# Kernel optimization log

Hardware: AMD Instinct MI355X
Metric: run time of the kernel (lower is better)

The kernel has to match this reference:

```python
import jax, jax.numpy as jnp
import numpy as np

N_HEAD = 16


def setup_inputs() -> dict:
    key = jax.random.key(0)
    ks = jax.random.split(key, 6)
    B, T, C = 2, 2048, 1024
    x = jax.random.normal(ks[0], (B, T, C), dtype=jnp.float32)
    # causal mask, broadcastable over [B, H, T, T]
    attn_mask = jnp.tril(jnp.ones((T, T), dtype=jnp.int32))[None, None]
    s = 1.0 / np.sqrt(C)
    W_attn = jax.random.normal(ks[1], (C, 3 * C), dtype=jnp.float32) * s
    b_attn = jnp.zeros((3 * C,), dtype=jnp.float32)
    W_proj = jax.random.normal(ks[2], (C, C), dtype=jnp.float32) * s
    b_proj = jnp.zeros((C,), dtype=jnp.float32)
    return {"x": x, "attn_mask": attn_mask, "W_attn": W_attn,
            "b_attn": b_attn, "W_proj": W_proj, "b_proj": b_proj}


def reference(x, attn_mask, W_attn, b_attn, W_proj, b_proj):
    B, T, C = x.shape
    H = N_HEAD
    D = C // H
    qkv = x @ W_attn + b_attn                      # [B, T, 3C]
    q, k, v = jnp.split(qkv, 3, axis=-1)
    q = q.reshape(B, T, H, D).transpose(0, 2, 1, 3)  # [B, H, T, D]
    k = k.reshape(B, T, H, D).transpose(0, 2, 1, 3)
    v = v.reshape(B, T, H, D).transpose(0, 2, 1, 3)
    att = jnp.einsum('bhtd,bhsd->bhts', q, k) * (1.0 / np.sqrt(D))
    att = jnp.where(attn_mask == 0, jnp.float32(-jnp.inf), att)
    att = jax.nn.softmax(att, axis=-1)             # [B, H, T, T]
    y = jnp.einsum('bhts,bhsd->bhtd', att, v)      # [B, H, T, D]
    y = y.transpose(0, 2, 1, 3).reshape(B, T, C)
    y = y @ W_proj + b_proj
    return y
```

## Files before the change

### kernel.cpp

```cpp
#include <hip/hip_runtime.h>
#include <hip/hip_bf16.h>
#include <stdint.h>

#define H_NUM 16
#define DH 64
#define TSEQ 2048
#define CDIM 1024

typedef short shortx8 __attribute__((ext_vector_type(8)));
typedef float f32x4 __attribute__((ext_vector_type(4)));
typedef unsigned short u16;
typedef unsigned int u32;
typedef unsigned long long u64;

#define MFMA16(a,b,c) __builtin_amdgcn_mfma_f32_16x16x32_bf16(a,b,c,0,0,0)

static __device__ __forceinline__ u16 f2bf(float f) {
  union { float f; u32 u; } v; v.f = f;
  u32 r = v.u + 0x7fffu + ((v.u >> 16) & 1u);
  return (u16)(r >> 16);
}
static __device__ __forceinline__ float bf2f(u16 b) {
  union { u32 u; float f; } v; v.u = ((u32)b) << 16;
  return v.f;
}

static __device__ __forceinline__ void gload_lds16(const void* g, void* l) {
  __builtin_amdgcn_global_load_lds(
    (const __attribute__((address_space(1))) void*)g,
    (__attribute__((address_space(3))) void*)l, 16, 0, 0);
}

extern "C" __global__ __launch_bounds__(1024) void k_prep(
    const float* __restrict__ x, u16* __restrict__ xb,
    const float* __restrict__ Wa, u16* __restrict__ wat,
    const float* __restrict__ Wp, u16* __restrict__ wpt)
{
  __shared__ float t[32][33];
  int bid = blockIdx.x, tid = threadIdx.x;
  if (bid < 1024) {
    int i = bid * 1024 + tid;
    float4 v = ((const float4*)x)[i];
    union { u16 h[4]; uint2 u; } o;
    o.h[0] = f2bf(v.x); o.h[1] = f2bf(v.y); o.h[2] = f2bf(v.z); o.h[3] = f2bf(v.w);
    ((uint2*)xb)[i] = o.u;
    return;
  }
  const float* in; u16* out; int Ccols, bx, by;
  if (bid < 4096) { int tt = bid - 1024; in = Wa; out = wat; Ccols = 3072; bx = tt % 96; by = tt / 96; }
  else            { int tt = bid - 4096; in = Wp; out = wpt; Ccols = 1024; bx = tt & 31; by = tt >> 5; }
  int tx = tid & 31, ty = tid >> 5;
  int c0 = bx * 32, r0 = by * 32;
  t[ty][tx] = in[(size_t)(r0 + ty) * Ccols + c0 + tx];
  __syncthreads();
  out[(size_t)(c0 + ty) * 1024 + r0 + tx] = f2bf(t[tx][ty]);
}

template<int OUT_BF16>
__global__ __launch_bounds__(256) void k_gemm_bt(
    const u16* __restrict__ A, const u16* __restrict__ Bt,
    const float* __restrict__ bias, void* __restrict__ Cout,
    int M, int N, int K)
{
  __shared__ u16 lds_a[2][128 * 32];
  __shared__ u16 lds_b[2][128 * 32];
  int tid = threadIdx.x;
  int w = tid >> 6, l = tid & 63;
  int lg = l >> 4, lr = l & 15;
  int nwg = gridDim.x * gridDim.y;
  int lin = blockIdx.y * gridDim.x + blockIdx.x;
  int cpx = nwg >> 3;
  int swz = (lin & 7) * cpx + (lin >> 3);
  int m0 = (swz / gridDim.x) * 128, n0 = (swz % gridDim.x) * 128;
  int wm = w >> 1, wn = w & 1;
  f32x4 acc[4][4];
#pragma unroll
  for (int i = 0; i < 4; ++i)
#pragma unroll
    for (int j = 0; j < 4; ++j) acc[i][j] = (f32x4){0.f, 0.f, 0.f, 0.f};

  auto STAGE = [&](int k0, int buf) {
#pragma unroll
    for (int j = 0; j < 2; ++j) {
      int ci = w * 2 + j;
      gload_lds16(A  + (size_t)(m0 + ci * 16 + (l >> 2)) * K + k0 + (l & 3) * 8,
                  (char*)lds_a[buf] + ci * 1024);
      gload_lds16(Bt + (size_t)(n0 + ci * 16 + (l >> 2)) * K + k0 + (l & 3) * 8,
                  (char*)lds_b[buf] + ci * 1024);
    }
  };

  int nt = K >> 5;
  STAGE(0, 0);
  int cur = 0;
  for (int t = 0; t < nt; ++t) {
    asm volatile("s_waitcnt vmcnt(0)" ::: "memory");
    __syncthreads();
    if (t + 1 < nt) STAGE((t + 1) << 5, cur ^ 1);
    shortx8 af[4], bf[4];
#pragma unroll
    for (int i = 0; i < 4; ++i) {
      af[i] = *(const shortx8*)((const char*)lds_a[cur] + (64 * wm + 16 * i + lr) * 64 + lg * 16);
      bf[i] = *(const shortx8*)((const char*)lds_b[cur] + (64 * wn + 16 * i + lr) * 64 + lg * 16);
    }
    __builtin_amdgcn_s_setprio(1);
#pragma unroll
    for (int mi = 0; mi < 4; ++mi)
#pragma unroll
      for (int ni = 0; ni < 4; ++ni)
        acc[mi][ni] = MFMA16(af[mi], bf[ni], acc[mi][ni]);
    __builtin_amdgcn_s_setprio(0);
    cur ^= 1;
  }
#pragma unroll
  for (int mi = 0; mi < 4; ++mi)
#pragma unroll
    for (int ni = 0; ni < 4; ++ni) {
      int col = n0 + 64 * wn + 16 * ni + lr;
      float bz = bias[col];
#pragma unroll
      for (int r = 0; r < 4; ++r) {
        int row = m0 + 64 * wm + 16 * mi + 4 * lg + r;
        float v = acc[mi][ni][r] + bz;
        if (OUT_BF16) ((u16*)Cout)[(size_t)row * N + col] = f2bf(v);
        else          ((float*)Cout)[(size_t)row * N + col] = v;
      }
    }
}

extern "C" __global__ __launch_bounds__(256) void k_transpose_v(
    const u16* __restrict__ qkv, u16* __restrict__ vt)
{
  __shared__ u16 tile[64][72];
  int bh = blockIdx.y; int b = bh >> 4, h = bh & 15;
  int t0 = blockIdx.x * 64;
  int tid = threadIdx.x;
#pragma unroll
  for (int p = 0; p < 2; ++p) {
    int tr = p * 32 + (tid >> 3), dc = (tid & 7) * 8;
    shortx8 v = *(const shortx8*)(qkv + (size_t)(b * TSEQ + t0 + tr) * 3072 + 2 * CDIM + h * DH + dc);
    *(shortx8*)&tile[tr][dc] = v;
  }
  __syncthreads();
#pragma unroll
  for (int p = 0; p < 2; ++p) {
    int dr = p * 32 + (tid >> 3), tc = (tid & 7) * 8;
    shortx8 o;
#pragma unroll
    for (int j = 0; j < 8; ++j) o[j] = (short)tile[tc + j][dr];
    *(shortx8*)(vt + (size_t)(bh * DH + dr) * TSEQ + t0 + tc) = o;
  }
}

extern "C" __global__ __launch_bounds__(256) void k_attn(
    const u16* __restrict__ qkv, const u16* __restrict__ vt, u16* __restrict__ yb)
{
  __shared__ u16 lds_k[2][64 * 64];
  __shared__ u16 lds_v[2][64 * 64];
  __shared__ u16 lds_p[4 * 1024];
  int d = blockIdx.x;
  int xcd = d & 7, j = d >> 3;
  int hb = xcd + 8 * (j >> 4);
  int bx = j & 15;
  int h = hb & 15, b = hb >> 4;
  int tid = threadIdx.x, w = tid >> 6, l = tid & 63;
  int lg = l >> 4, lr = l & 15;
  const float QSCALE = 0.18033688011112042f;
  const u16* vbase = vt + (size_t)(b * H_NUM + h) * DH * TSEQ;
  u16* pw = lds_p + w * 1024;

  auto STAGE = [&](int kv0, int buf) {
#pragma unroll
    for (int jj = 0; jj < 2; ++jj) {
      int ci = w * 2 + jj;
      int row = ci * 8 + (l >> 3);
      int a = ((l & 7) ^ (row & 7)) * 8;
      gload_lds16(qkv + (size_t)(b * TSEQ + kv0 + row) * 3072 + CDIM + h * DH + a,
                  (char*)lds_k[buf] + ci * 1024);
      gload_lds16(vbase + (size_t)row * TSEQ + kv0 + a,
                  (char*)lds_v[buf] + ci * 1024);
    }
  };

  for (int qi = 0; qi < 2; ++qi) {
    int qb = qi ? (31 - bx) : bx;
    int q0 = qb * 64;

    int qrow = q0 + 16 * w + lr;
    const u16* qp = qkv + (size_t)(b * TSEQ + qrow) * 3072 + h * DH;
    shortx8 qf[2];
#pragma unroll
    for (int s = 0; s < 2; ++s) {
      shortx8 v = *(const shortx8*)(qp + s * 32 + lg * 8);
#pragma unroll
      for (int i = 0; i < 8; ++i) v[i] = (short)f2bf(bf2f((u16)v[i]) * QSCALE);
      qf[s] = v;
    }

    f32x4 yacc[4];
#pragma unroll
    for (int i = 0; i < 4; ++i) yacc[i] = (f32x4){0.f, 0.f, 0.f, 0.f};
    float m_run[4] = {-3.0e38f, -3.0e38f, -3.0e38f, -3.0e38f};
    float l_part[4] = {0.f, 0.f, 0.f, 0.f};

    int nt = qb + 1;
    __syncthreads();
    STAGE(0, 0);
    int cur = 0;
    for (int t = 0; t < nt; ++t) {
      int kv0 = t * 64;
      asm volatile("s_waitcnt vmcnt(0)" ::: "memory");
      __syncthreads();
      if (t + 1 < nt) STAGE(kv0 + 64, cur ^ 1);

      f32x4 s[4];
#pragma unroll
      for (int idx = 0; idx < 4; ++idx) s[idx] = (f32x4){0.f, 0.f, 0.f, 0.f};
      int kswz = (lr & 7) << 4;
      __builtin_amdgcn_s_setprio(1);
#pragma unroll
      for (int idx = 0; idx < 4; ++idx) {
        const char* kb = (const char*)lds_k[cur] + (idx * 16 + lr) * 128;
#pragma unroll
        for (int d0 = 0; d0 < 2; ++d0) {
          shortx8 kf = *(const shortx8*)(kb + ((d0 * 64 + lg * 16) ^ kswz));
          s[idx] = MFMA16(qf[d0], kf, s[idx]);
        }
      }
      __builtin_amdgcn_s_setprio(0);
      if (kv0 == q0) {
#pragma unroll
        for (int idx = 0; idx < 4; ++idx)
#pragma unroll
          for (int r = 0; r < 4; ++r) {
            int row_l = 16 * w + 4 * lg + r;
            if (idx * 16 + lr > row_l) s[idx][r] = -3.0e38f;
          }
      }

#pragma unroll
      for (int r = 0; r < 4; ++r) {
        float a0 = s[0][r], a1 = s[1][r], a2 = s[2][r], a3 = s[3][r];
        float pmax = fmaxf(fmaxf(a0, a1), fmaxf(a2, a3));
        float mr = m_run[r];
        u64 bal = __ballot(pmax > mr + 8.0f);
        if ((bal >> (lg * 16)) & 0xFFFFull) {
          float gm = pmax;
          gm = fmaxf(gm, __shfl_xor(gm, 1));
          gm = fmaxf(gm, __shfl_xor(gm, 2));
          gm = fmaxf(gm, __shfl_xor(gm, 4));
          gm = fmaxf(gm, __shfl_xor(gm, 8));
          float mn = fmaxf(mr, gm);
          float al = __builtin_amdgcn_exp2f(mr - mn);
          l_part[r] *= al;
#pragma unroll
          for (int dt = 0; dt < 4; ++dt) yacc[dt][r] *= al;
          m_run[r] = mn; mr = mn;
        }
        float p0 = __builtin_amdgcn_exp2f(a0 - mr);
        float p1 = __builtin_amdgcn_exp2f(a1 - mr);
        float p2 = __builtin_amdgcn_exp2f(a2 - mr);
        float p3 = __builtin_amdgcn_exp2f(a3 - mr);
        l_part[r] += (p0 + p1) + (p2 + p3);
        u32 pk01, pk23;
        asm("v_cvt_pk_bf16_f32 %0, %1, %2" : "=v"(pk01) : "v"(p0), "v"(p1));
        asm("v_cvt_pk_bf16_f32 %0, %1, %2" : "=v"(pk23) : "v"(p2), "v"(p3));
        int q = 4 * lg + r;
        int rb = q * 64, swq = (q & 7) << 3;
        pw[rb + ((lr)      ^ swq)] = (u16)pk01;
        pw[rb + ((16 + lr) ^ swq)] = (u16)(pk01 >> 16);
        pw[rb + ((32 + lr) ^ swq)] = (u16)pk23;
        pw[rb + ((48 + lr) ^ swq)] = (u16)(pk23 >> 16);
      }
      asm volatile("s_waitcnt lgkmcnt(0)" ::: "memory");
      __builtin_amdgcn_sched_barrier(0);

      int pswz = (lr & 7) << 4;
      __builtin_amdgcn_s_setprio(1);
#pragma unroll
      for (int c = 0; c < 2; ++c) {
        shortx8 pa = *(const shortx8*)((const char*)pw + lr * 128 + ((c * 64 + lg * 16) ^ pswz));
#pragma unroll
        for (int dt = 0; dt < 4; ++dt) {
          int vr = dt * 16 + lr;
          shortx8 vf = *(const shortx8*)((const char*)lds_v[cur] + vr * 128 +
                         ((c * 64 + lg * 16) ^ ((vr & 7) << 4)));
          yacc[dt] = MFMA16(pa, vf, yacc[dt]);
        }
      }
      __builtin_amdgcn_s_setprio(0);
      cur ^= 1;
    }

#pragma unroll
    for (int r = 0; r < 4; ++r) {
      float lsum = l_part[r];
      lsum += __shfl_xor(lsum, 1);
      lsum += __shfl_xor(lsum, 2);
      lsum += __shfl_xor(lsum, 4);
      lsum += __shfl_xor(lsum, 8);
      float inv = 1.0f / lsum;
      int row = q0 + 16 * w + 4 * lg + r;
      u16* yp = yb + (size_t)(b * TSEQ + row) * CDIM + h * DH;
#pragma unroll
      for (int dt = 0; dt < 4; ++dt)
        yp[dt * 16 + lr] = f2bf(yacc[dt][r] * inv);
    }
  }
}

extern "C" void kernel_launch(void* const* d_in, const int* in_sizes, int n_in,
                              void* d_out, int out_size, void* d_ws, size_t ws_size,
                              hipStream_t stream) {
  const float* x      = (const float*)d_in[0];
  const float* W_attn = (const float*)d_in[2];
  const float* b_attn = (const float*)d_in[3];
  const float* W_proj = (const float*)d_in[4];
  const float* b_proj = (const float*)d_in[5];

  char* ws = (char*)d_ws;
  u16* xb  = (u16*)ws;
  u16* wat = (u16*)(ws + (8ull  << 20));
  u16* wpt = (u16*)(ws + (14ull << 20));
  u16* qkv = (u16*)(ws + (16ull << 20));
  u16* vt  = (u16*)(ws + (40ull << 20));
  u16* yb  = (u16*)(ws + (48ull << 20));

  k_prep<<<dim3(5120), dim3(1024), 0, stream>>>(x, xb, W_attn, wat, W_proj, wpt);
  k_gemm_bt<1><<<dim3(24, 32), dim3(256), 0, stream>>>(xb, wat, b_attn, qkv, 4096, 3072, 1024);
  k_transpose_v<<<dim3(32, 32), dim3(256), 0, stream>>>(qkv, vt);
  k_attn<<<dim3(512), dim3(256), 0, stream>>>(qkv, vt, yb);
  k_gemm_bt<0><<<dim3(8, 32), dim3(256), 0, stream>>>(yb, wpt, b_proj, d_out, 4096, 1024, 1024);
}
```

Measured before the change: 128.5 us.

## Software-pipeline attention loop: overlap next tile's QK^T with current PV

Restructures the flash-attention inner loop so that the QK^T MFMAs for tile t+1 are issued together with the PV MFMAs for tile t, with the softmax for the next tile done afterwards. K/V staging moves from double to triple buffering so that loads for tile t+2 can be in flight while two tiles are resident. The aim is to hide softmax and LDS latency behind matrix work and to cut the stalls between dependent phases. In exchange, LDS use per block rises from about 40KB to 56KB, which can lower the number of resident blocks per CU, and the explicit lgkmcnt wait between the P writes and the PV reads is removed.

```diff
diff --git a/kernel.cpp b/kernel.cpp
--- a/kernel.cpp
+++ b/kernel.cpp
@@ -155,8 +155,8 @@
 extern "C" __global__ __launch_bounds__(256) void k_attn(
     const u16* __restrict__ qkv, const u16* __restrict__ vt, u16* __restrict__ yb)
 {
-  __shared__ u16 lds_k[2][64 * 64];
-  __shared__ u16 lds_v[2][64 * 64];
+  __shared__ u16 lds_k[3][64 * 64];
+  __shared__ u16 lds_v[3][64 * 64];
   __shared__ u16 lds_p[4 * 1024];
   int d = blockIdx.x;
   int xcd = d & 7, j = d >> 3;
@@ -190,11 +190,11 @@
     const u16* qp = qkv + (size_t)(b * TSEQ + qrow) * 3072 + h * DH;
     shortx8 qf[2];
 #pragma unroll
-    for (int s = 0; s < 2; ++s) {
-      shortx8 v = *(const shortx8*)(qp + s * 32 + lg * 8);
+    for (int s_ = 0; s_ < 2; ++s_) {
+      shortx8 v = *(const shortx8*)(qp + s_ * 32 + lg * 8);
 #pragma unroll
       for (int i = 0; i < 8; ++i) v[i] = (short)f2bf(bf2f((u16)v[i]) * QSCALE);
-      qf[s] = v;
+      qf[s_] = v;
     }
 
     f32x4 yacc[4];
@@ -202,32 +202,24 @@
     for (int i = 0; i < 4; ++i) yacc[i] = (f32x4){0.f, 0.f, 0.f, 0.f};
     float m_run[4] = {-3.0e38f, -3.0e38f, -3.0e38f, -3.0e38f};
     float l_part[4] = {0.f, 0.f, 0.f, 0.f};
-
-    int nt = qb + 1;
-    __syncthreads();
-    STAGE(0, 0);
-    int cur = 0;
-    for (int t = 0; t < nt; ++t) {
-      int kv0 = t * 64;
-      asm volatile("s_waitcnt vmcnt(0)" ::: "memory");
-      __syncthreads();
-      if (t + 1 < nt) STAGE(kv0 + 64, cur ^ 1);
-
-      f32x4 s[4];
+    f32x4 s[4];
+
+    auto QKT = [&](int buf) {
 #pragma unroll
       for (int idx = 0; idx < 4; ++idx) s[idx] = (f32x4){0.f, 0.f, 0.f, 0.f};
       int kswz = (lr & 7) << 4;
-      __builtin_amdgcn_s_setprio(1);
 #pragma unroll
       for (int idx = 0; idx < 4; ++idx) {
-        const char* kb = (const char*)lds_k[cur] + (idx * 16 + lr) * 128;
+        const char* kb_ = (const char*)lds_k[buf] + (idx * 16 + lr) * 128;
 #pragma unroll
         for (int d0 = 0; d0 < 2; ++d0) {
-          shortx8 kf = *(const shortx8*)(kb + ((d0 * 64 + lg * 16) ^ kswz));
+          shortx8 kf = *(const shortx8*)(kb_ + ((d0 * 64 + lg * 16) ^ kswz));
           s[idx] = MFMA16(qf[d0], kf, s[idx]);
         }
       }
-      __builtin_amdgcn_s_setprio(0);
+    };
+
+    auto SOFTMAX = [&](int kv0) {
       if (kv0 == q0) {
 #pragma unroll
         for (int idx = 0; idx < 4; ++idx)
@@ -237,7 +229,6 @@
             if (idx * 16 + lr > row_l) s[idx][r] = -3.0e38f;
           }
       }
-
 #pragma unroll
       for (int r = 0; r < 4; ++r) {
         float a0 = s[0][r], a1 = s[1][r], a2 = s[2][r], a3 = s[3][r];
@@ -272,24 +263,47 @@
         pw[rb + ((32 + lr) ^ swq)] = (u16)pk23;
         pw[rb + ((48 + lr) ^ swq)] = (u16)(pk23 >> 16);
       }
-      asm volatile("s_waitcnt lgkmcnt(0)" ::: "memory");
-      __builtin_amdgcn_sched_barrier(0);
-
+    };
+
+    auto PV = [&](int buf) {
       int pswz = (lr & 7) << 4;
-      __builtin_amdgcn_s_setprio(1);
 #pragma unroll
       for (int c = 0; c < 2; ++c) {
         shortx8 pa = *(const shortx8*)((const char*)pw + lr * 128 + ((c * 64 + lg * 16) ^ pswz));
 #pragma unroll
         for (int dt = 0; dt < 4; ++dt) {
           int vr = dt * 16 + lr;
-          shortx8 vf = *(const shortx8*)((const char*)lds_v[cur] + vr * 128 +
+          shortx8 vf = *(const shortx8*)((const char*)lds_v[buf] + vr * 128 +
                          ((c * 64 + lg * 16) ^ ((vr & 7) << 4)));
           yacc[dt] = MFMA16(pa, vf, yacc[dt]);
         }
       }
+    };
+
+    int nt = qb + 1;
+    __syncthreads();
+    STAGE(0, 0);
+    asm volatile("s_waitcnt vmcnt(0)" ::: "memory");
+    __syncthreads();
+    __builtin_amdgcn_s_setprio(1);
+    QKT(0);
+    __builtin_amdgcn_s_setprio(0);
+    if (nt > 1) STAGE(64, 1);
+    SOFTMAX(0);
+
+    int vb = 0;
+    for (int t = 0; t < nt; ++t) {
+      int kb = vb + 1; if (kb == 3) kb = 0;
+      int st = kb + 1; if (st == 3) st = 0;
+      asm volatile("s_waitcnt vmcnt(0)" ::: "memory");
+      __syncthreads();
+      __builtin_amdgcn_s_setprio(1);
+      if (t + 1 < nt) QKT(kb);
+      PV(vb);
       __builtin_amdgcn_s_setprio(0);
-      cur ^= 1;
+      if (t + 2 < nt) STAGE((t + 2) * 64, st);
+      if (t + 1 < nt) SOFTMAX((t + 1) * 64);
+      vb = kb;
     }
 
 #pragma unroll
```

After: 127.0 us. About the same (-1.2%).
